# Optimization experiments

Measured on AMD Instinct MI355X. Metric: run time of the kernel, lower is better.

The kernel has to match this reference:

```python
import jax, jax.numpy as jnp
import numpy as np

N_PTS, N_NODES, N_EDGES, N_CMP = 512, 10000, 50000, 64
# edge types produced by _get_edge_states, plus NULL (do_include_null=True, do_include_all_16=False)
EDGE_TYPES = jnp.array([0, 2, 3, 5, 9], dtype=jnp.int32)  # NULL, NOR, NCONV, NIMPL, AND
N_TYPES = 5
# mapping of temp = 2*a+b in {0,1,2,3} -> edge-type code
TEMP_TO_CODE = jnp.array([2, 3, 5, 9], dtype=jnp.int32)  # NOR, NCONV, NIMPL, AND


def _edge_to_logical(es):
    # es: (n, E) int codes -> (n, N_TYPES*E) bool, type-major layout matching
    # torch.permute([1,0,2]).reshape(n, n_types*n_edges)
    oh = es[:, None, :] == EDGE_TYPES[None, :, None]  # (n, N_TYPES, E)
    return oh.reshape(es.shape[0], N_TYPES * es.shape[1])


def setup_inputs() -> dict:
    key = jax.random.key(0)
    k1, k2, k3 = jax.random.split(key, 3)
    node_activations = jax.random.randint(k1, (N_PTS, N_NODES), 0, 2, dtype=jnp.int32)
    edge_endnode_idx = jax.random.randint(k2, (N_EDGES, 2), 0, N_NODES, dtype=jnp.int32)
    # learned edge states: random categorical over the 5 reachable types
    learned_type_idx = jax.random.randint(k3, (N_CMP, N_EDGES), 0, N_TYPES, dtype=jnp.int32)
    learned_codes = EDGE_TYPES[learned_type_idx]
    binarized_learned = _edge_to_logical(learned_codes).astype(jnp.float32)  # (N_CMP, 5*E)
    return {
        "node_activations": node_activations,
        "binarized_learned": binarized_learned,
        "edge_endnode_idx": edge_endnode_idx,
    }


def reference(node_activations, binarized_learned, edge_endnode_idx):
    # gather endpoint activations: (n_pts, n_edges)
    a = node_activations[:, edge_endnode_idx[:, 0]]
    b = node_activations[:, edge_endnode_idx[:, 1]]
    temp = 2 * a + b  # in {0,1,2,3}
    code = TEMP_TO_CODE[temp]  # edge_type_filter is empty -> no filtering
    # one-hot encode edge states: (n_pts, 5*n_edges)
    bact = _edge_to_logical(code).astype(binarized_learned.dtype)
    # energies: (n_pts, n_cmp); torch does int8 matmul of the same 0/1 values
    energies = jnp.einsum('ck,nk->nc', binarized_learned, bact)
    return energies - jnp.min(energies)
```

## Files before the change

kernel.cpp:

```cpp
#include <hip/hip_runtime.h>
#include <stdint.h>

#define N_PTS   512
#define N_NODES 10000
#define N_EDGES 50000
#define N_CMP   64
#define W64     784
#define EBITS   (W64 * 64)
#define LSTRIDE (N_CMP * W64)
#define NCHUNK  49
#define CW      16
#define TN      16
#define NGRP    (N_PTS / TN)
#define BST_ROW 10016
#define NB_BST  ((N_NODES + 255) / 256)
#define NBLK_L  (NCHUNK * N_CMP)

typedef unsigned long long u64;

__global__ void build_all(const int* __restrict__ act, const float* __restrict__ BL,
                          u64* __restrict__ Lp, uint16_t* __restrict__ bsT) {
    int bid = blockIdx.x;
    int t = threadIdx.x;
    if (bid < NBLK_L) {
        __shared__ uint16_t sh[256];
        int c = bid / NCHUNK, bx = bid % NCHUNK;
        int e0 = bx * 1024 + 4 * t;
        int nla = 0, nlb = 0, ntz = 0xF;
        if (e0 < N_EDGES) {
            const float* base = BL + (size_t)c * (5 * N_EDGES) + e0;
            float4 p0 = *(const float4*)(base);
            float4 p2 = *(const float4*)(base + 2 * N_EDGES);
            float4 p3 = *(const float4*)(base + 3 * N_EDGES);
            float4 p4 = *(const float4*)(base + 4 * N_EDGES);
            #define B_(f) ((f) != 0.f ? 1 : 0)
            nla = (B_(p3.x) | B_(p4.x)) | ((B_(p3.y) | B_(p4.y)) << 1)
                | ((B_(p3.z) | B_(p4.z)) << 2) | ((B_(p3.w) | B_(p4.w)) << 3);
            nlb = (B_(p2.x) | B_(p4.x)) | ((B_(p2.y) | B_(p4.y)) << 1)
                | ((B_(p2.z) | B_(p4.z)) << 2) | ((B_(p2.w) | B_(p4.w)) << 3);
            ntz = B_(p0.x) | (B_(p0.y) << 1) | (B_(p0.z) << 2) | (B_(p0.w) << 3);
            #undef B_
        }
        sh[t] = (uint16_t)(nla | (nlb << 4) | (ntz << 8));
        __syncthreads();
        if (t < 48) {
            int p = t >> 4, w = t & 15;
            const u64* v = (const u64*)sh + w * 4;
            u64 word = 0;
            #pragma unroll
            for (int i = 0; i < 4; ++i) {
                u64 x = v[i];
                #pragma unroll
                for (int kk = 0; kk < 4; ++kk)
                    word |= ((x >> (16 * kk + 4 * p)) & 0xFULL) << (4 * (i * 4 + kk));
            }
            Lp[(size_t)p * LSTRIDE + (size_t)c * W64 + bx * 16 + w] = word;
        }
    } else {
        int rem = bid - NBLK_L;
        int g = rem / NB_BST, nb = rem % NB_BST;
        int node = nb * 256 + t;
        if (node < N_NODES) {
            uint32_t m = 0;
            #pragma unroll
            for (int p = 0; p < TN; ++p)
                m |= (act[(size_t)(g * TN + p) * N_NODES + node] != 0 ? 1u : 0u) << p;
            bsT[(size_t)g * BST_ROW + node] = (uint16_t)m;
        }
    }
}

__global__ void __launch_bounds__(512, 6)
match_fused(const u64* __restrict__ Lp, const uint16_t* __restrict__ bsT,
            const int2* __restrict__ edges, uint32_t* __restrict__ part32) {
    __shared__ u64 Ll[3][CW][65];
    __shared__ __align__(16) uint16_t bsTl[BST_ROW];

    int chunk = blockIdx.x;
    int g = blockIdx.y;
    int t = threadIdx.x;
    int lane = t & 63;
    int wave = t >> 6;
    int cw0 = chunk * CW;

    {
        int w = t & 15;
        #pragma unroll
        for (int pass = 0; pass < 6; ++pass) {
            int r = pass * 32 + (t >> 4);
            int plane = r >> 6, c = r & 63;
            Ll[plane][w][c] = Lp[(size_t)plane * LSTRIDE + (size_t)c * W64 + cw0 + w];
        }
    }
    {
        const uint4* src = (const uint4*)(bsT + (size_t)g * BST_ROW);
        uint4* dst = (uint4*)bsTl;
        for (int idx = t; idx < BST_ROW / 8; idx += 512) dst[idx] = src[idx];
    }
    __syncthreads();

    uint32_t cnt[TN];
    #pragma unroll
    for (int p = 0; p < TN; ++p) cnt[p] = 0;

    #pragma unroll
    for (int j = 0; j < 2; ++j) {
        int w = wave * 2 + j;
        int2 cur = edges[min(chunk * 1024 + w * 64 + lane, N_EDGES - 1)];
        uint32_t a16 = bsTl[cur.x];
        uint32_t b16 = bsTl[cur.y];
        u64 la = Ll[0][w][lane];
        u64 lb = Ll[1][w][lane];
        u64 tz = Ll[2][w][lane];
        #pragma unroll
        for (int p = 0; p < TN; ++p) {
            u64 A = __ballot((a16 >> p) & 1);
            u64 B = __ballot((b16 >> p) & 1);
            cnt[p] += __popcll(tz | (la ^ A) | (lb ^ B));
        }
    }

    __syncthreads();
    uint32_t (*red32)[8][64] = (uint32_t (*)[8][64])bsTl;
    #pragma unroll
    for (int q = 0; q < 8; ++q)
        red32[wave][q][lane] = cnt[2 * q] | (cnt[2 * q + 1] << 16);
    __syncthreads();
    {
        int q = t >> 6, c = t & 63;
        uint32_t s = 0;
        #pragma unroll
        for (int wv = 0; wv < 8; ++wv) s += red32[wv][q][c];
        part32[(((size_t)chunk * NGRP + g) * 8 + q) * 64 + c] = s;
    }
}

__global__ void reduce1(const uint32_t* __restrict__ part32, int* __restrict__ energy,
                        int* __restrict__ blockmin) {
    int t = blockIdx.x * 256 + threadIdx.x;
    int c = t & 63, n = t >> 6;
    int g = n >> 4, p = n & 15;
    int q = p >> 1, hi = (p & 1) * 16;
    int s = 0;
    #pragma unroll 7
    for (int ch = 0; ch < NCHUNK; ++ch)
        s += (part32[(((size_t)ch * NGRP + g) * 8 + q) * 64 + c] >> hi) & 0xFFFF;
    int e = EBITS - s;
    energy[t] = e;
    int m = e;
    for (int off = 32; off; off >>= 1) m = min(m, __shfl_down(m, off, 64));
    __shared__ int wm[4];
    if ((threadIdx.x & 63) == 0) wm[threadIdx.x >> 6] = m;
    __syncthreads();
    if (threadIdx.x == 0) blockmin[blockIdx.x] = min(min(wm[0], wm[1]), min(wm[2], wm[3]));
}

__global__ void subk(const int* __restrict__ energy, const int* __restrict__ blockmin,
                     float* __restrict__ out) {
    __shared__ int wm[4];
    __shared__ int ms;
    int t = threadIdx.x;
    int m = t < 128 ? blockmin[t] : 0x7fffffff;
    for (int off = 32; off; off >>= 1) m = min(m, __shfl_down(m, off, 64));
    if ((t & 63) == 0) wm[t >> 6] = m;
    __syncthreads();
    if (t == 0) ms = min(wm[0], wm[1]);
    __syncthreads();
    int mv = ms;
    int i = blockIdx.x * 256 + t;
    int4 e = ((const int4*)energy)[i];
    ((float4*)out)[i] = make_float4((float)(e.x - mv), (float)(e.y - mv),
                                    (float)(e.z - mv), (float)(e.w - mv));
}

extern "C" void kernel_launch(void* const* d_in, const int* in_sizes, int n_in,
                              void* d_out, int out_size, void* d_ws, size_t ws_size,
                              hipStream_t stream) {
    const int*   act   = (const int*)d_in[0];
    const float* BL    = (const float*)d_in[1];
    const int2*  edges = (const int2*)d_in[2];
    float* out = (float*)d_out;

    u64* Lp = (u64*)d_ws;
    uint16_t* bsT = (uint16_t*)(Lp + 3 * (size_t)LSTRIDE);
    uint32_t* part32 = (uint32_t*)(bsT + (size_t)NGRP * BST_ROW);
    int* energy   = (int*)(part32 + (size_t)NCHUNK * NGRP * 8 * 64);
    int* blockmin = energy + N_PTS * N_CMP;

    build_all   <<<NBLK_L + NGRP * NB_BST, 256, 0, stream>>>(act, BL, Lp, bsT);
    match_fused <<<dim3(NCHUNK, NGRP), 512, 0, stream>>>(Lp, bsT, edges, part32);
    reduce1     <<<N_PTS * N_CMP / 256, 256, 0, stream>>>(part32, energy, blockmin);
    subk        <<<N_PTS * N_CMP / 1024, 256, 0, stream>>>(energy, blockmin, out);
}
```

Before: 40.77 us.

## Accumulate chunk partials with atomics and fuse reduction into one finalize kernel

The per-chunk partial count buffer and its separate reduction pass are replaced by atomicAdd of packed 16-bit counts into a small zeroed accumulator, which build_all clears. The two-kernel reduce/min/subtract tail becomes one finalize kernel in which every block redundantly scans the accumulator for the global max match count, then writes energies as max minus count. This removes one launch and the 49-chunk partial traffic, in exchange for atomic contention across chunks and redundant max scans per block. It relies on packed 16-bit halves never overflowing into each other.

```diff
diff --git a/kernel.cpp b/kernel.cpp
--- a/kernel.cpp
+++ b/kernel.cpp
@@ -15,13 +15,16 @@
 #define BST_ROW 10016
 #define NB_BST  ((N_NODES + 255) / 256)
 #define NBLK_L  (NCHUNK * N_CMP)
+#define E32SZ   (NGRP * 8 * 64)
 
 typedef unsigned long long u64;
 
 __global__ void build_all(const int* __restrict__ act, const float* __restrict__ BL,
-                          u64* __restrict__ Lp, uint16_t* __restrict__ bsT) {
+                          u64* __restrict__ Lp, uint16_t* __restrict__ bsT,
+                          uint32_t* __restrict__ energy32) {
     int bid = blockIdx.x;
     int t = threadIdx.x;
+    if (bid < E32SZ / 256) energy32[bid * 256 + t] = 0;
     if (bid < NBLK_L) {
         __shared__ uint16_t sh[256];
         int c = bid / NCHUNK, bx = bid % NCHUNK;
@@ -72,7 +75,7 @@
 
 __global__ void __launch_bounds__(512, 6)
 match_fused(const u64* __restrict__ Lp, const uint16_t* __restrict__ bsT,
-            const int2* __restrict__ edges, uint32_t* __restrict__ part32) {
+            const int2* __restrict__ edges, uint32_t* __restrict__ energy32) {
     __shared__ u64 Ll[3][CW][65];
     __shared__ __align__(16) uint16_t bsTl[BST_ROW];
 
@@ -131,46 +134,38 @@
         uint32_t s = 0;
         #pragma unroll
         for (int wv = 0; wv < 8; ++wv) s += red32[wv][q][c];
-        part32[(((size_t)chunk * NGRP + g) * 8 + q) * 64 + c] = s;
+        atomicAdd(&energy32[(g * 8 + q) * 64 + c], s);
     }
 }
 
-__global__ void reduce1(const uint32_t* __restrict__ part32, int* __restrict__ energy,
-                        int* __restrict__ blockmin) {
-    int t = blockIdx.x * 256 + threadIdx.x;
-    int c = t & 63, n = t >> 6;
-    int g = n >> 4, p = n & 15;
-    int q = p >> 1, hi = (p & 1) * 16;
-    int s = 0;
-    #pragma unroll 7
-    for (int ch = 0; ch < NCHUNK; ++ch)
-        s += (part32[(((size_t)ch * NGRP + g) * 8 + q) * 64 + c] >> hi) & 0xFFFF;
-    int e = EBITS - s;
-    energy[t] = e;
-    int m = e;
-    for (int off = 32; off; off >>= 1) m = min(m, __shfl_down(m, off, 64));
-    __shared__ int wm[4];
-    if ((threadIdx.x & 63) == 0) wm[threadIdx.x >> 6] = m;
-    __syncthreads();
-    if (threadIdx.x == 0) blockmin[blockIdx.x] = min(min(wm[0], wm[1]), min(wm[2], wm[3]));
-}
-
-__global__ void subk(const int* __restrict__ energy, const int* __restrict__ blockmin,
-                     float* __restrict__ out) {
+__global__ void finalize(const uint32_t* __restrict__ energy32, float* __restrict__ out) {
     __shared__ int wm[4];
     __shared__ int ms;
     int t = threadIdx.x;
-    int m = t < 128 ? blockmin[t] : 0x7fffffff;
-    for (int off = 32; off; off >>= 1) m = min(m, __shfl_down(m, off, 64));
-    if ((t & 63) == 0) wm[t >> 6] = m;
+    int mx = 0;
+    const uint4* e4 = (const uint4*)energy32;
+    for (int i = t; i < E32SZ / 4; i += 256) {
+        uint4 v = e4[i];
+        mx = max(mx, (int)(v.x & 0xFFFF)); mx = max(mx, (int)(v.x >> 16));
+        mx = max(mx, (int)(v.y & 0xFFFF)); mx = max(mx, (int)(v.y >> 16));
+        mx = max(mx, (int)(v.z & 0xFFFF)); mx = max(mx, (int)(v.z >> 16));
+        mx = max(mx, (int)(v.w & 0xFFFF)); mx = max(mx, (int)(v.w >> 16));
+    }
+    for (int off = 32; off; off >>= 1) mx = max(mx, __shfl_down(mx, off, 64));
+    if ((t & 63) == 0) wm[t >> 6] = mx;
     __syncthreads();
-    if (t == 0) ms = min(wm[0], wm[1]);
+    if (t == 0) ms = max(max(wm[0], wm[1]), max(wm[2], wm[3]));
     __syncthreads();
-    int mv = ms;
-    int i = blockIdx.x * 256 + t;
-    int4 e = ((const int4*)energy)[i];
-    ((float4*)out)[i] = make_float4((float)(e.x - mv), (float)(e.y - mv),
-                                    (float)(e.z - mv), (float)(e.w - mv));
+    int mxv = ms;
+    #pragma unroll
+    for (int k = 0; k < 4; ++k) {
+        int o = blockIdx.x * 1024 + k * 256 + t;
+        int n = o >> 6, c = o & 63;
+        int g = n >> 4, p = n & 15, q = p >> 1, h = p & 1;
+        uint32_t w = energy32[(g * 8 + q) * 64 + c];
+        int s = (int)((w >> (16 * h)) & 0xFFFF);
+        out[o] = (float)(mxv - s);
+    }
 }
 
 extern "C" void kernel_launch(void* const* d_in, const int* in_sizes, int n_in,
@@ -183,12 +178,9 @@
 
     u64* Lp = (u64*)d_ws;
     uint16_t* bsT = (uint16_t*)(Lp + 3 * (size_t)LSTRIDE);
-    uint32_t* part32 = (uint32_t*)(bsT + (size_t)NGRP * BST_ROW);
-    int* energy   = (int*)(part32 + (size_t)NCHUNK * NGRP * 8 * 64);
-    int* blockmin = energy + N_PTS * N_CMP;
+    uint32_t* energy32 = (uint32_t*)(bsT + (size_t)NGRP * BST_ROW);
 
-    build_all   <<<NBLK_L + NGRP * NB_BST, 256, 0, stream>>>(act, BL, Lp, bsT);
-    match_fused <<<dim3(NCHUNK, NGRP), 512, 0, stream>>>(Lp, bsT, edges, part32);
-    reduce1     <<<N_PTS * N_CMP / 256, 256, 0, stream>>>(part32, energy, blockmin);
-    subk        <<<N_PTS * N_CMP / 1024, 256, 0, stream>>>(energy, blockmin, out);
+    build_all   <<<NBLK_L + NGRP * NB_BST, 256, 0, stream>>>(act, BL, Lp, bsT, energy32);
+    match_fused <<<dim3(NCHUNK, NGRP), 512, 0, stream>>>(Lp, bsT, edges, energy32);
+    finalize    <<<32, 256, 0, stream>>>(energy32, out);
 }
```

Result: no change. 40.36 us (-1.0%).
